# Kernel tuning notes

Measured on AMD Instinct MI355X. Metric: run time of the kernel, lower is better.

## Reference

```python
import jax, jax.numpy as jnp
import numpy as np

DIM = 1024
IMG_H, IMG_W = 512, 1408
CROP = 224
IMAGE_ORDER = (2, 0, 1, 5, 3, 4)
B, NC, NB = 2, 6, 32


def setup_inputs():
    key = jax.random.key(0)
    ks = jax.random.split(key, 12)
    camera_imgs = jax.random.normal(ks[0], (B, NC, 3, IMG_H, IMG_W), jnp.float32)
    u = jax.random.uniform(ks[1], (B, NB, 9), dtype=jnp.float32)
    centers = jnp.stack([u[..., 0] * 45.0 + 5.0,
                         (u[..., 1] - 0.5) * 40.0,
                         (u[..., 2] - 0.5) * 4.0], -1)
    pred_boxes = jnp.concatenate([centers, u[..., 3:] * 2.0], -1)  # [B,NB,9]
    K = np.array([[500., 0., IMG_W / 2.], [0., 500., IMG_H / 2.], [0., 0., 1.]])
    R_l2c = np.array([[0., -1., 0.], [0., 0., -1.], [1., 0., 0.]])  # lidar->camera axes
    mats = np.zeros((NC, 4, 4), np.float32)
    for c in range(NC):
        yaw = 2.0 * np.pi * c / NC
        Rz = np.array([[np.cos(yaw), -np.sin(yaw), 0.], [np.sin(yaw), np.cos(yaw), 0.], [0., 0., 1.]])
        mats[c, :3, :3] = K @ R_l2c @ Rz.T
        mats[c, 3, 3] = 1.0
    lidar2image = jnp.broadcast_to(jnp.asarray(mats), (B, NC, 4, 4))
    eye4 = jnp.eye(4, dtype=jnp.float32)
    img_aug_matrix = jnp.broadcast_to(eye4, (B, NC, 4, 4))
    lidar_aug_matrix = jnp.broadcast_to(eye4, (B, 4, 4))
    momentum = jnp.float32(0.5)
    box_default_dim = jax.random.normal(ks[2], (1, DIM), jnp.float32)
    theta_w = jnp.zeros((4, 9), jnp.float32)  # zero-init as in torch code
    theta_b = jnp.array([1., 0., 0., 1.], jnp.float32)

    def cw(k, shape):
        fan = shape[1] * shape[2] * shape[3]
        return jax.random.normal(k, shape, jnp.float32) * (2.0 / fan) ** 0.5
    conv1 = cw(ks[3], (64, 3, 7, 7))
    conv2 = cw(ks[4], (256, 64, 3, 3))
    conv3 = cw(ks[5], (DIM, 256, 3, 3))
    pos_embed = jax.random.normal(ks[6], (50, DIM), jnp.float32) * 0.02
    s = DIM ** -0.5
    wq = jax.random.normal(ks[7], (DIM, DIM), jnp.float32) * s
    wk = jax.random.normal(ks[8], (DIM, DIM), jnp.float32) * s
    wv = jax.random.normal(ks[9], (DIM, DIM), jnp.float32) * s
    wo = jax.random.normal(ks[10], (DIM, DIM), jnp.float32) * s
    return dict(camera_imgs=camera_imgs, pred_boxes=pred_boxes,
                img_aug_matrix=img_aug_matrix, lidar_aug_matrix=lidar_aug_matrix,
                lidar2image=lidar2image, momentum=momentum,
                box_default_dim=box_default_dim, theta_w=theta_w, theta_b=theta_b,
                conv1=conv1, conv2=conv2, conv3=conv3, pos_embed=pos_embed,
                wq=wq, wk=wk, wv=wv, wo=wo)


def _project(pred_boxes, lidar_aug_matrix, lidar2image, img_aug_matrix):
    # returns vu [B,NC,NB,2] = (row, col) pixel coords, on_img [B,NC,NB]
    def per_b(boxes, la, l2i, aug):
        c = boxes[:, :3] - la[:3, 3]                       # [NB,3]
        c = jnp.linalg.inv(la[:3, :3]) @ c.T               # [3,NB]
        c = l2i[:, :3, :3] @ c + l2i[:, :3, 3:4]           # [NC,3,NB]
        z = jnp.clip(c[:, 2], 1e-5, 1e5)
        xy = c[:, :2] / z[:, None]
        c = jnp.concatenate([xy, z[:, None]], 1)
        c = aug[:, :3, :3] @ c + aug[:, :3, 3:4]
        uv = c[:, :2].transpose(0, 2, 1)                   # [NC,NB,2] (col,row)
        vu = uv[..., ::-1]                                 # (row,col)
        on = (vu[..., 0] < IMG_H) & (vu[..., 0] >= 0) & (vu[..., 1] < IMG_W) & (vu[..., 1] >= 0)
        return vu, on
    return jax.vmap(per_b)(pred_boxes, lidar_aug_matrix, lidar2image, img_aug_matrix)


def _base_grid(h, w):
    # torch affine_grid align_corners=False pixel-center coords
    xs = (2.0 * jnp.arange(w) + 1.0) / w - 1.0
    ys = (2.0 * jnp.arange(h) + 1.0) / h - 1.0
    gx, gy = jnp.meshgrid(xs, ys)  # [h,w]
    return jnp.stack([gx, gy, jnp.ones_like(gx)], -1)  # [h,w,3]


def _grid_sample(img, grid):
    # img [C,H,W]; grid [...,2] xy in [-1,1]; bilinear, zeros padding, align_corners=False
    C, H, W = img.shape
    ix = ((grid[..., 0] + 1.0) * W - 1.0) / 2.0
    iy = ((grid[..., 1] + 1.0) * H - 1.0) / 2.0
    x0 = jnp.floor(ix); y0 = jnp.floor(iy)
    x1 = x0 + 1.0; y1 = y0 + 1.0
    wx = ix - x0; wy = iy - y0

    def gather(xx, yy):
        xi = jnp.clip(xx, 0, W - 1).astype(jnp.int32)
        yi = jnp.clip(yy, 0, H - 1).astype(jnp.int32)
        valid = (xx >= 0) & (xx <= W - 1) & (yy >= 0) & (yy <= H - 1)
        return img[:, yi, xi] * valid.astype(img.dtype)  # [C, ...]
    v00 = gather(x0, y0); v01 = gather(x1, y0)
    v10 = gather(x0, y1); v11 = gather(x1, y1)
    return (v00 * (1 - wx) * (1 - wy) + v01 * wx * (1 - wy)
            + v10 * (1 - wx) * wy + v11 * wx * wy)  # [C, ...]


def _clip_head(x, conv1, conv2, conv3, pos_embed, wq, wk, wv, wo):
    dn = ('NCHW', 'OIHW', 'NCHW')
    h = jax.nn.relu(jax.lax.conv_general_dilated(x, conv1, (4, 4), 'SAME', dimension_numbers=dn))
    h = jax.nn.relu(jax.lax.conv_general_dilated(h, conv2, (4, 4), 'SAME', dimension_numbers=dn))
    h = jax.nn.relu(jax.lax.conv_general_dilated(h, conv3, (2, 2), 'SAME', dimension_numbers=dn))  # [M,D,7,7]
    tok = h.reshape(h.shape[0], DIM, 49).transpose(0, 2, 1)              # [M,49,D]
    tok = jnp.concatenate([tok.mean(1, keepdims=True), tok], 1) + pos_embed  # [M,50,D]
    q = tok[:, :1] @ wq
    k = tok @ wk
    v = tok @ wv
    attn = jax.nn.softmax((q @ k.transpose(0, 2, 1)) * (DIM ** -0.5), -1)
    return ((attn @ v) @ wo)[:, 0]  # [M,D]


def reference(camera_imgs, pred_boxes, img_aug_matrix, lidar_aug_matrix, lidar2image,
              momentum, box_default_dim, theta_w, theta_b,
              conv1, conv2, conv3, pos_embed, wq, wk, wv, wo):
    N = B * NB
    vu, on_img = _project(pred_boxes, lidar_aug_matrix, lidar2image, img_aug_matrix)  # [B,NC,NB,2],[B,NC,NB]
    boxes_flat = pred_boxes.reshape(N, 9)
    rot = jnp.tanh(boxes_flat @ theta_w.T + theta_b).reshape(N, 2, 2)   # theta_rot MLP
    ty = vu[..., 0] / IMG_H * 2.0 - 1.0                                 # [B,NC,NB]
    tx = vu[..., 1] / IMG_W * 2.0 - 1.0
    pos = jnp.stack([tx, ty], -1).transpose(0, 2, 1, 3).reshape(N, NC, 2)
    theta = jnp.concatenate([jnp.broadcast_to(rot[:, None], (N, NC, 2, 2)),
                             pos[..., None]], -1)                        # [N,NC,2,3]
    base = _base_grid(CROP, CROP)                                        # [224,224,3]
    grids = jnp.einsum('hwk,ncjk->nchwj', base, theta)                   # [N,NC,224,224,2]
    grids = grids.reshape(B, NB, NC, CROP, CROP, 2)
    crops = []
    for b in range(B):
        for c in range(NC):
            smp = _grid_sample(camera_imgs[b, c], grids[b, :, c])        # [3,NB,224,224]
            crops.append(smp.transpose(1, 0, 2, 3))
    crops = jnp.stack(crops).reshape(B, NC, NB, 3, CROP, CROP)
    crops = crops.transpose(0, 2, 1, 3, 4, 5).reshape(N * NC, 3, CROP, CROP)
    emb = _clip_head(crops, conv1, conv2, conv3, pos_embed, wq, wk, wv, wo).reshape(N, NC, DIM)
    valid = on_img.transpose(0, 2, 1).reshape(N, NC)
    e = jnp.broadcast_to(box_default_dim, (N, DIM))
    for c in IMAGE_ORDER:  # sequential EMA over cameras, skipping off-image ones
        m = valid[:, c:c + 1]
        e = jnp.where(m, momentum * e + (1.0 - momentum) * emb[:, c], e)
    return e  # [N, DIM]
```

## Files before the change

kernel.cpp:

```cpp
#include <hip/hip_runtime.h>
#include <hip/hip_bf16.h>

#define DIMN 1024
#define IMG_H 512
#define IMG_W 1408
#define CROPN 224
#define NCAM 6
#define NBOXB 32
#define NBOX 64
#define NIMG 384

typedef __hip_bfloat16 bf16;
typedef unsigned short u16;
typedef float f32x4 __attribute__((ext_vector_type(4)));
typedef short bf16x8 __attribute__((ext_vector_type(8)));
typedef u16 u16x4 __attribute__((ext_vector_type(4)));
typedef u16 u16x8 __attribute__((ext_vector_type(8)));

__device__ __forceinline__ float b2f(bf16 x) { return __bfloat162float(x); }
__device__ __forceinline__ u16 f2us(float x) {
  bf16 h = __float2bfloat16(x);
  return *(u16*)&h;
}
__device__ __forceinline__ bf16x8 as_b(u16x8 x) {
  union { u16x8 u; bf16x8 b; } c; c.u = x; return c.b;
}

__global__ void k_w1r(const float* __restrict__ in, u16* __restrict__ out) {
  int idx = blockIdx.x * 256 + threadIdx.x;
  if (idx >= 64 * 224) return;
  int oc = idx / 224, t = idx % 224;
  int r = t >> 5, u = t & 31, kw = u >> 2, ch = u & 3;
  u16 v = (kw < 7 && ch < 3) ? f2us(in[((oc * 3 + ch) * 7 + r) * 7 + kw]) : (u16)0;
  out[(((oc >> 4) * 28 + (t >> 3)) * 16 + (oc & 15)) * 8 + (t & 7)] = v;
}
__global__ void k_w2r(const float* __restrict__ in, u16* __restrict__ out) {
  int idx = blockIdx.x * 256 + threadIdx.x;
  if (idx >= 256 * 576) return;
  int oc = idx / 576, t = idx % 576;
  int rk = t >> 6, ic = t & 63, r = rk / 3, kw = rk % 3;
  u16 v = f2us(in[((oc * 64 + ic) * 3 + r) * 3 + kw]);
  out[(((oc >> 4) * 72 + (t >> 3)) * 16 + (oc & 15)) * 8 + (t & 7)] = v;
}
__global__ void k_w3r(const float* __restrict__ in, u16* __restrict__ out) {
  int idx = blockIdx.x * 256 + threadIdx.x;
  if (idx >= 1024 * 2304) return;
  int oc = idx / 2304, t = idx % 2304;
  int rk = t >> 8, ic = t & 255, r = rk / 3, kw = rk % 3;
  u16 v = f2us(in[((oc * 256 + ic) * 3 + r) * 3 + kw]);
  int ocb = oc >> 4, mm = oc & 15, kb = t >> 3, kj = t & 7;
  out[(((size_t)ocb * 288 + kb) * 16 + mm) * 8 + kj] = v;
}
__global__ void k_transpose_t(const float* __restrict__ w, float* __restrict__ wt) {
  __shared__ float tile[32][33];
  int x = blockIdx.x * 32 + threadIdx.x;
  for (int j = threadIdx.y; j < 32; j += 8)
    tile[j][threadIdx.x] = w[(size_t)(blockIdx.y * 32 + j) * 1024 + x];
  __syncthreads();
  int x2 = blockIdx.y * 32 + threadIdx.x;
  for (int j = threadIdx.y; j < 32; j += 8)
    wt[(size_t)(blockIdx.x * 32 + j) * 1024 + x2] = tile[threadIdx.x][j];
}

__global__ void k_proj(const float* __restrict__ boxes, const float* __restrict__ la_m,
                       const float* __restrict__ l2i, const float* __restrict__ aug,
                       const float* __restrict__ tw, const float* __restrict__ tb,
                       float* __restrict__ theta_out, int* __restrict__ valid_out) {
  int t = threadIdx.x;
  if (t >= NIMG) return;
  int n = t / NCAM, cam = t % NCAM;
  int b = n / NBOXB, nb = n % NBOXB;

  float la[4][4];
  for (int r = 0; r < 4; r++)
    for (int c = 0; c < 4; c++) la[r][c] = la_m[b * 16 + r * 4 + c];
  float a00=la[0][0],a01=la[0][1],a02=la[0][2];
  float a10=la[1][0],a11=la[1][1],a12=la[1][2];
  float a20=la[2][0],a21=la[2][1],a22=la[2][2];
  float c00 =  a11*a22 - a12*a21;
  float c01 = -(a10*a22 - a12*a20);
  float c02 =  a10*a21 - a11*a20;
  float det = a00*c00 + a01*c01 + a02*c02;
  float id = 1.0f / det;
  float inv[3][3];
  inv[0][0] = c00*id;                 inv[0][1] = -(a01*a22-a02*a21)*id;  inv[0][2] =  (a01*a12-a02*a11)*id;
  inv[1][0] = c01*id;                 inv[1][1] =  (a00*a22-a02*a20)*id;  inv[1][2] = -(a00*a12-a02*a10)*id;
  inv[2][0] = c02*id;                 inv[2][1] = -(a00*a21-a01*a20)*id;  inv[2][2] =  (a00*a11-a01*a10)*id;

  float bx[9];
  for (int i = 0; i < 9; i++) bx[i] = boxes[(b * NBOXB + nb) * 9 + i];
  float c0[3] = { bx[0]-la[0][3], bx[1]-la[1][3], bx[2]-la[2][3] };
  float c1[3];
  for (int r = 0; r < 3; r++) c1[r] = inv[r][0]*c0[0] + inv[r][1]*c0[1] + inv[r][2]*c0[2];

  const float* M = l2i + (size_t)(b * NCAM + cam) * 16;
  float p[3];
  for (int r = 0; r < 3; r++)
    p[r] = M[r*4+0]*c1[0] + M[r*4+1]*c1[1] + M[r*4+2]*c1[2] + M[r*4+3];
  float z = fminf(fmaxf(p[2], 1e-5f), 100000.0f);
  float x = p[0] / z, y = p[1] / z;
  const float* A = aug + (size_t)(b * NCAM + cam) * 16;
  float u = A[0]*x + A[1]*y + A[2]*z + A[3];
  float v = A[4]*x + A[5]*y + A[6]*z + A[7];

  int on = (v < (float)IMG_H) && (v >= 0.0f) && (u < (float)IMG_W) && (u >= 0.0f);
  float ty = v / (float)IMG_H * 2.0f - 1.0f;
  float tx = u / (float)IMG_W * 2.0f - 1.0f;

  float s[4];
  for (int j = 0; j < 4; j++) {
    float acc = tb[j];
    for (int i = 0; i < 9; i++) acc += tw[j * 9 + i] * bx[i];
    s[j] = tanhf(acc);
  }
  float* o = theta_out + t * 6;
  o[0] = s[0]; o[1] = s[1]; o[2] = tx;
  o[3] = s[2]; o[4] = s[3]; o[5] = ty;
  valid_out[t] = on;
}

#define HALO_PX 1356
__global__ void k_zero_halo(u16x4* __restrict__ c) {
  int t = blockIdx.x * 256 + threadIdx.x;
  int i = t / HALO_PX;
  if (i >= NIMG) return;
  int r = t % HALO_PX;
  int ph, pw;
  if (r < 684) {
    int rr = r / 228;
    ph = (rr == 0) ? 0 : (rr == 1 ? 225 : 226);
    pw = r % 228;
  } else {
    int q = r - 684;
    ph = 1 + q / 3;
    int s = q % 3;
    pw = (s == 0) ? 0 : (s == 1 ? 225 : 226);
  }
  c[(size_t)i * 228 * 228 + ph * 228 + pw] = (u16x4){0, 0, 0, 0};
}

__global__ __launch_bounds__(256) void k_sample(const float* __restrict__ imgs,
                                                const float* __restrict__ theta,
                                                u16* __restrict__ crops) {
  int idx = blockIdx.x * 256 + threadIdx.x;
  int i = idx / (CROPN * CROPN);
  int rem = idx - i * (CROPN * CROPN);
  int yy = rem / CROPN, xx = rem % CROPN;
  const float* th = theta + i * 6;
  float gx = (2.0f * xx + 1.0f) / (float)CROPN - 1.0f;
  float gy = (2.0f * yy + 1.0f) / (float)CROPN - 1.0f;
  float grid_x = th[0]*gx + th[1]*gy + th[2];
  float grid_y = th[3]*gx + th[4]*gy + th[5];
  float ix = ((grid_x + 1.0f) * (float)IMG_W - 1.0f) * 0.5f;
  float iy = ((grid_y + 1.0f) * (float)IMG_H - 1.0f) * 0.5f;
  float x0 = floorf(ix), y0 = floorf(iy);
  float wx = ix - x0, wy = iy - y0;
  int cam = i % NCAM, b = i / (NBOXB * NCAM);
  const float* base = imgs + (size_t)(b * NCAM + cam) * 3 * IMG_H * IMG_W;

  float xf[2] = { x0, x0 + 1.0f };
  float yf[2] = { y0, y0 + 1.0f };
  float wxa[2] = { 1.0f - wx, wx };
  float wya[2] = { 1.0f - wy, wy };
  int   xi[2], yi[2], vx[2], vy[2];
  for (int j = 0; j < 2; j++) {
    vx[j] = (xf[j] >= 0.0f) && (xf[j] <= (float)(IMG_W - 1));
    vy[j] = (yf[j] >= 0.0f) && (yf[j] <= (float)(IMG_H - 1));
    xi[j] = (int)fminf(fmaxf(xf[j], 0.0f), (float)(IMG_W - 1));
    yi[j] = (int)fminf(fmaxf(yf[j], 0.0f), (float)(IMG_H - 1));
  }
  float res[3];
  #pragma unroll
  for (int ch = 0; ch < 3; ch++) {
    const float* cp = base + (size_t)ch * IMG_H * IMG_W;
    float r = 0.0f;
    #pragma unroll
    for (int jy = 0; jy < 2; jy++)
      #pragma unroll
      for (int jx = 0; jx < 2; jx++) {
        float val = (vx[jx] && vy[jy]) ? cp[yi[jy] * IMG_W + xi[jx]] : 0.0f;
        r += val * wxa[jx] * wya[jy];
      }
    res[ch] = r;
  }
  u16x4 st = { f2us(res[0]), f2us(res[1]), f2us(res[2]), 0 };
  *(u16x4*)(crops + ((size_t)i * 228 * 228 + (size_t)(yy + 1) * 228 + (xx + 1)) * 4) = st;
}


#define C1_GROUPS 34
__global__ __launch_bounds__(256) void k_conv1m(const u16* __restrict__ X,
                                                const u16* __restrict__ W,
                                                u16* __restrict__ out) {
  __shared__ u16x8 sX[C1_GROUPS * 64];
  int blk = blockIdx.x;
  int i = blk / 14, rg = blk % 14;
  int tid = threadIdx.x, wv = tid >> 6, lane = tid & 63;
  int m = lane & 15, quad = lane >> 4;

  const u16* src = X + ((size_t)i * 51984 + (size_t)(rg * 16) * 228) * 4;
  #pragma unroll
  for (int j = 0; j < 9; j++) {
    int g = wv + j * 4;
    if (g < C1_GROUPS) {
      int c = g * 64 + lane;
      int cc = c < 2166 ? c : 2165;
      __builtin_amdgcn_global_load_lds(
          (const __attribute__((address_space(1))) void*)(src + (size_t)cc * 8),
          (__attribute__((address_space(3))) void*)(sX + g * 64),
          16, 0, 0);
    }
  }
  __syncthreads();

  int col[4];
  #pragma unroll
  for (int nt = 0; nt < 4; nt++) col[nt] = nt * 16 + m;
  f32x4 acc[4][4];
  #pragma unroll
  for (int t = 0; t < 4; t++)
    #pragma unroll
    for (int nt = 0; nt < 4; nt++) acc[t][nt] = (f32x4){0.f, 0.f, 0.f, 0.f};

  #pragma unroll
  for (int r = 0; r < 7; r++) {
    bf16x8 a[4];
    #pragma unroll
    for (int t = 0; t < 4; t++)
      a[t] = as_b(*(const u16x8*)(W + (size_t)(((t * 28 + r * 4 + quad) * 16 + m) * 8)));
    int lrow = wv * 4 + r;
    #pragma unroll
    for (int nt = 0; nt < 4; nt++) {
      int cl = col[nt] < 56 ? col[nt] : 55;
      bf16x8 bfr = as_b(sX[lrow * 114 + cl * 2 + quad]);
      #pragma unroll
      for (int t = 0; t < 4; t++)
        acc[t][nt] = __builtin_amdgcn_mfma_f32_16x16x32_bf16(a[t], bfr, acc[t][nt], 0, 0, 0);
    }
  }
  int oh = rg * 4 + wv;
  #pragma unroll
  for (int nt = 0; nt < 4; nt++) {
    if (col[nt] < 56) {
      int n = oh * 56 + col[nt];
      #pragma unroll
      for (int t = 0; t < 4; t++) {
        u16x4 st;
        #pragma unroll
        for (int r4 = 0; r4 < 4; r4++) st[r4] = f2us(fmaxf(acc[t][nt][r4], 0.f));
        *(u16x4*)(out + ((size_t)i * 3136 + n) * 64 + t * 16 + quad * 4) = st;
      }
    }
  }
}

__global__ __launch_bounds__(256, 3) void k_conv2m(const u16* __restrict__ X,
                                                   const u16* __restrict__ W,
                                                   u16* __restrict__ out) {
  __shared__ u16x8 s2[3136];
  int bid = blockIdx.x;
  int i = bid / 7, ohg = bid % 7;
  int tid = threadIdx.x, wv = tid >> 6, lane = tid & 63;
  int m = lane & 15, quad = lane >> 4;

  const u16* src = X + ((size_t)i * 3136 + 8 * ohg * 56) * 64;
  u16x8 tmp[13];
  #pragma unroll
  for (int j = 0; j < 13; j++) {
    int c = tid + j * 256;
    int cc = c < 3136 ? c : 3135;
    tmp[j] = *(const u16x8*)(src + (size_t)cc * 8);
  }
  #pragma unroll
  for (int j = 0; j < 13; j++) {
    int c = tid + j * 256;
    int cc = c < 3136 ? c : 3135;
    int pixel = cc >> 3;
    int li = pixel / 56, iw = pixel - li * 56;
    int g = (14 * (li >> 2) + (iw >> 2)) & 15;
    s2[(cc & ~15) | ((cc ^ g) & 15)] = tmp[j];
  }
  __syncthreads();

  int nl[2], pk2[9][2];
  #pragma unroll
  for (int nt = 0; nt < 2; nt++) {
    int n = nt * 16 + m;
    nl[nt] = n;
    int nc = n < 28 ? n : 27;
    int ohl = nc / 14, ow = nc - ohl * 14;
    int g = nc & 15;
    #pragma unroll
    for (int rk = 0; rk < 9; rk++) {
      int r = rk / 3, kw = rk % 3;
      int pixel = (ohl * 4 + r) * 56 + (ow * 4 + kw);
      int cb = pixel * 8;
      int base2 = (cb & ~15) | ((cb & 8) ^ (g & 8));
      pk2[rk][nt] = base2 | (g & 7);
    }
  }
  f32x4 acc[4][2];
  #pragma unroll
  for (int t = 0; t < 4; t++)
    #pragma unroll
    for (int nt = 0; nt < 2; nt++) acc[t][nt] = (f32x4){0.f, 0.f, 0.f, 0.f};

  const u16* wbase = W + (size_t)(wv * 4) * (72 * 128) + m * 8;
  auto loadA = [&](int t, int s) {
    return as_b(*(const u16x8*)(wbase + (size_t)(t * 72 + s * 4 + quad) * 128));
  };
  auto loadB = [&](int nt, int s) {
    int pkv = pk2[s >> 1][nt];
    int sub = (s & 1) * 4 + quad;
    return as_b(s2[(pkv & ~7) | (sub ^ (pkv & 7))]);
  };

  bf16x8 A_[3][4], B_[3][2];
  #pragma unroll
  for (int t = 0; t < 4; t++) { A_[0][t] = loadA(t, 0); A_[1][t] = loadA(t, 1); }
  #pragma unroll
  for (int nt = 0; nt < 2; nt++) { B_[0][nt] = loadB(nt, 0); B_[1][nt] = loadB(nt, 1); }

  #pragma unroll
  for (int s = 0; s < 18; s++) {
    if (s + 2 < 18) {
      #pragma unroll
      for (int t = 0; t < 4; t++) A_[(s + 2) % 3][t] = loadA(t, s + 2);
      #pragma unroll
      for (int nt = 0; nt < 2; nt++) B_[(s + 2) % 3][nt] = loadB(nt, s + 2);
    }
    #pragma unroll
    for (int nt = 0; nt < 2; nt++)
      #pragma unroll
      for (int t = 0; t < 4; t++)
        acc[t][nt] = __builtin_amdgcn_mfma_f32_16x16x32_bf16(A_[s % 3][t], B_[s % 3][nt], acc[t][nt], 0, 0, 0);
  }

  #pragma unroll
  for (int nt = 0; nt < 2; nt++) {
    if (nl[nt] < 28) {
      int n = ohg * 28 + nl[nt];
      #pragma unroll
      for (int t = 0; t < 4; t++) {
        u16x4 st;
        #pragma unroll
        for (int r4 = 0; r4 < 4; r4++) st[r4] = f2us(fmaxf(acc[t][nt][r4], 0.f));
        *(u16x4*)(out + ((size_t)i * 196 + n) * 256 + wv * 64 + t * 16 + quad * 4) = st;
      }
    }
  }
}

__global__ __launch_bounds__(512, 2) void k_conv3m(const u16* __restrict__ X,
                                                   const u16* __restrict__ W,
                                                   float* __restrict__ out3) {
  __shared__ u16x8 sX8[6688];
  int bid = blockIdx.x;
  int og = (bid >> 2) & 1;
  int i  = (bid >> 3) * 4 + (bid & 3);
  int tid = threadIdx.x;
  int wv = tid >> 6, lane = tid & 63;

  const u16* src = X + (size_t)i * (196 * 256);
  #pragma unroll
  for (int j = 0; j < 13; j++) {
    int gi = (j < 12) ? (wv + j * 8) : (96 + wv);
    if (j < 12 || wv < 2) {
      int slot = gi * 64 + lane;
      int p = slot >> 5;
      int ih = p / 14, iw = p - ih * 14;
      int g = (7 * (ih >> 1) + (iw >> 1)) & 15;
      int c = (slot & ~15) | ((slot ^ g) & 15);
      __builtin_amdgcn_global_load_lds(
          (const __attribute__((address_space(1))) void*)(src + (size_t)c * 8),
          (__attribute__((address_space(3))) void*)(sX8 + gi * 64),
          16, 0, 0);
    }
  }
  if (tid < 32) sX8[6656 + tid] = (u16x8){0,0,0,0,0,0,0,0};
  __syncthreads();

  int m = lane & 15, quad = lane >> 4;
  int ocw = og * 512 + wv * 64;
  int narr[4], oh2[4], ow2[4];
  #pragma unroll
  for (int nt = 0; nt < 4; nt++) {
    int n = nt * 16 + m;
    narr[nt] = n;
    int nc = n < 49 ? n : 48;
    int oh = nc / 7, ow = nc - oh * 7;
    oh2[nt] = oh * 2; ow2[nt] = ow * 2;
  }
  f32x4 acc[4][4];
  #pragma unroll
  for (int t = 0; t < 4; t++)
    #pragma unroll
    for (int nt = 0; nt < 4; nt++) acc[t][nt] = (f32x4){0.f, 0.f, 0.f, 0.f};

  const u16* wbase = W + (size_t)(ocw >> 4) * (288 * 128) + m * 8;

  int bc[4], bk[4];
  auto set_bparams = [&](int rk) {
    const int r = rk / 3, kw = rk % 3;
    #pragma unroll
    for (int nt = 0; nt < 4; nt++) {
      int ih = oh2[nt] + r, iw = ow2[nt] + kw;
      bool valid = (narr[nt] < 49) && (ih < 14) && (iw < 14);
      int p = ih * 14 + iw;
      bc[nt] = valid ? p * 32 : 6656;
      bk[nt] = valid ? ((7 * (ih >> 1) + (iw >> 1)) & 15) : 0;
    }
  };
  auto loadA = [&](int t, int s) {
    return as_b(*(const u16x8*)(wbase + (size_t)(t * 288 + 4 * s + quad) * 128));
  };
  auto loadB = [&](int nt, int q4) {
    return as_b(sX8[bc[nt] + ((q4 + quad) ^ bk[nt])]);
  };

  bf16x8 A_[3][4], B_[2][4];
  set_bparams(0);
  #pragma unroll
  for (int t = 0; t < 4; t++) {
    A_[0][t] = loadA(t, 0);
    A_[1][t] = loadA(t, 1);
  }
  #pragma unroll
  for (int nt = 0; nt < 4; nt++) B_[0][nt] = loadB(nt, 0);

  #pragma unroll
  for (int s = 0; s < 72; s++) {
    if (s + 2 < 72) {
      #pragma unroll
      for (int t = 0; t < 4; t++) A_[(s + 2) % 3][t] = loadA(t, s + 2);
    }
    if (s + 1 < 72) {
      if (((s + 1) & 7) == 0) set_bparams((s + 1) >> 3);
      #pragma unroll
      for (int nt = 0; nt < 4; nt++) B_[(s + 1) & 1][nt] = loadB(nt, ((s + 1) & 7) * 4);
    }
    #pragma unroll
    for (int nt = 0; nt < 4; nt++)
      #pragma unroll
      for (int t = 0; t < 4; t++)
        acc[t][nt] = __builtin_amdgcn_mfma_f32_16x16x32_bf16(A_[s % 3][t], B_[s & 1][nt], acc[t][nt], 0, 0, 0);
  }

  #pragma unroll
  for (int nt = 0; nt < 4; nt++) {
    int n = narr[nt];
    if (n < 49) {
      #pragma unroll
      for (int t = 0; t < 4; t++) {
        f32x4 o;
        #pragma unroll
        for (int r4 = 0; r4 < 4; r4++) o[r4] = fmaxf(acc[t][nt][r4], 0.f);
        *(f32x4*)(out3 + ((size_t)i * 49 + n) * DIMN + ocw + t * 16 + quad * 4) = o;
      }
    }
  }
}

__global__ __launch_bounds__(256) void k_tok(const float* __restrict__ h,
                                             const float* __restrict__ pos,
                                             float* __restrict__ tok) {
  int blk = blockIdx.x;
  int i = blk / 50, t = blk % 50;
  int d = threadIdx.x * 4;
  float4 val;
  if (t == 0) {
    float sx = 0, sy = 0, sz = 0, sw = 0;
    for (int p = 0; p < 49; p++) {
      float4 v = *(const float4*)(h + ((size_t)i * 49 + p) * DIMN + d);
      sx += v.x; sy += v.y; sz += v.z; sw += v.w;
    }
    const float inv49 = 1.0f / 49.0f;
    val.x = sx * inv49; val.y = sy * inv49; val.z = sz * inv49; val.w = sw * inv49;
  } else {
    val = *(const float4*)(h + ((size_t)i * 49 + (t - 1)) * DIMN + d);
  }
  float4 pe = *(const float4*)(pos + (size_t)t * DIMN + d);
  float4 o; o.x = val.x + pe.x; o.y = val.y + pe.y; o.z = val.z + pe.z; o.w = val.w + pe.w;
  *(float4*)(tok + ((size_t)i * 50 + t) * DIMN + d) = o;
}

__global__ __launch_bounds__(256) void k_matvec2(const float* __restrict__ vecs, int vstride,
                                                 const float* __restrict__ M,
                                                 float* __restrict__ out) {
  __shared__ float s_v[4][DIMN];
  int i0 = blockIdx.x * 4;
  int h = blockIdx.y;
  for (int e = threadIdx.x; e < 4 * DIMN; e += 256)
    s_v[e >> 10][e & 1023] = vecs[(size_t)(i0 + (e >> 10)) * vstride + (e & 1023)];
  __syncthreads();
  int d0 = h * 512 + threadIdx.x * 2;
  float2 acc[4] = {{0,0},{0,0},{0,0},{0,0}};
  for (int e = 0; e < DIMN; e++) {
    float2 w = *(const float2*)(M + (size_t)e * DIMN + d0);
    #pragma unroll
    for (int im = 0; im < 4; im++) {
      float x = s_v[im][e];
      acc[im].x += x * w.x; acc[im].y += x * w.y;
    }
  }
  #pragma unroll
  for (int im = 0; im < 4; im++)
    *(float2*)(out + (size_t)(i0 + im) * DIMN + d0) = acc[im];
}

__global__ __launch_bounds__(256) void k_attn(const float* __restrict__ tok,
                                              const float* __restrict__ a1,
                                              float* __restrict__ tvec) {
  __shared__ float s_a[DIMN];
  __shared__ float s_sc[50];
  __shared__ float s_at[50];
  int i = blockIdx.x;
  for (int e = threadIdx.x; e < DIMN; e += 256) s_a[e] = a1[(size_t)i * DIMN + e];
  __syncthreads();
  int wave = threadIdx.x >> 6, lane = threadIdx.x & 63;
  for (int t = wave; t < 50; t += 4) {
    const float* tr = tok + ((size_t)i * 50 + t) * DIMN;
    float p = 0.0f;
    for (int mm = 0; mm < 16; mm++) {
      int e = lane + mm * 64;
      p += tr[e] * s_a[e];
    }
    for (int off = 32; off > 0; off >>= 1) p += __shfl_down(p, off, 64);
    if (lane == 0) s_sc[t] = p * 0.03125f;
  }
  __syncthreads();
  if (threadIdx.x == 0) {
    float mx = s_sc[0];
    for (int t = 1; t < 50; t++) mx = fmaxf(mx, s_sc[t]);
    float sum = 0.0f;
    for (int t = 0; t < 50; t++) { float ex = expf(s_sc[t] - mx); s_at[t] = ex; sum += ex; }
    float inv = 1.0f / sum;
    for (int t = 0; t < 50; t++) s_at[t] *= inv;
  }
  __syncthreads();
  int d0 = threadIdx.x * 4;
  float ax = 0, ay = 0, az = 0, aw = 0;
  for (int t = 0; t < 50; t++) {
    float at = s_at[t];
    float4 tv = *(const float4*)(tok + ((size_t)i * 50 + t) * DIMN + d0);
    ax += at * tv.x; ay += at * tv.y; az += at * tv.z; aw += at * tv.w;
  }
  float4 o; o.x = ax; o.y = ay; o.z = az; o.w = aw;
  *(float4*)(tvec + (size_t)i * DIMN + d0) = o;
}

__global__ void k_final(const float* __restrict__ emb,
                        const int* __restrict__ valid,
                        const float* __restrict__ bdd,
                        const float* __restrict__ momp,
                        float* __restrict__ out) {
  int n = blockIdx.x;
  int d0 = threadIdx.x * 4;
  float mom = momp[0];
  float e[4];
  #pragma unroll
  for (int j = 0; j < 4; j++) e[j] = bdd[d0 + j];
  const int order[6] = {2, 0, 1, 5, 3, 4};
  #pragma unroll
  for (int s = 0; s < 6; s++) {
    int c = order[s];
    int i = n * NCAM + c;
    if (valid[i]) {
      const float* er = emb + (size_t)i * DIMN + d0;
      #pragma unroll
      for (int j = 0; j < 4; j++) e[j] = mom * e[j] + (1.0f - mom) * er[j];
    }
  }
  #pragma unroll
  for (int j = 0; j < 4; j++) out[(size_t)n * DIMN + d0 + j] = e[j];
}

extern "C" void kernel_launch(void* const* d_in, const int* in_sizes, int n_in,
                              void* d_out, int out_size, void* d_ws, size_t ws_size,
                              hipStream_t stream) {
  const float* in_cam = (const float*)d_in[0];
  const float* in_box = (const float*)d_in[1];
  const float* in_aug = (const float*)d_in[2];
  const float* in_la  = (const float*)d_in[3];
  const float* in_l2i = (const float*)d_in[4];
  const float* in_mom = (const float*)d_in[5];
  const float* in_bdd = (const float*)d_in[6];
  const float* in_tw  = (const float*)d_in[7];
  const float* in_tb  = (const float*)d_in[8];
  const float* in_c1  = (const float*)d_in[9];
  const float* in_c2  = (const float*)d_in[10];
  const float* in_c3  = (const float*)d_in[11];
  const float* in_pe  = (const float*)d_in[12];
  const float* in_wq  = (const float*)d_in[13];
  const float* in_wk  = (const float*)d_in[14];
  const float* in_wv  = (const float*)d_in[15];
  const float* in_wo  = (const float*)d_in[16];

  char* base = (char*)d_ws;
  size_t off = 0;
  auto carve = [&](size_t bytes) -> char* {
    char* p = base + off;
    off += (bytes + 255) & ~(size_t)255;
    return p;
  };
  float* theta   = (float*)carve((size_t)NIMG * 6 * 4);
  int*   valid   = (int*)carve((size_t)NIMG * 4);
  float* qbuf    = (float*)carve((size_t)NIMG * DIMN * 4);
  float* a1buf   = (float*)carve((size_t)NIMG * DIMN * 4);
  float* tvbuf   = (float*)carve((size_t)NIMG * DIMN * 4);
  float* ctxbuf  = (float*)carve((size_t)NIMG * DIMN * 4);
  float* embbuf  = (float*)carve((size_t)NIMG * DIMN * 4);
  float* wkT_f   = (float*)carve((size_t)DIMN * DIMN * 4);
  u16*   W1r     = (u16*)carve((size_t)64 * 224 * 2);
  u16*   W2r     = (u16*)carve((size_t)256 * 576 * 2);
  u16*   W3r     = (u16*)carve((size_t)1024 * 2304 * 2);
  u16*   c2o     = (u16*)carve((size_t)NIMG * 196 * 256 * 2);
  char*  R1      = carve((size_t)NIMG * 228 * 228 * 4 * 2);
  u16*   c1o     = (u16*)carve((size_t)NIMG * 3136 * 64 * 2);
  u16*   crops   = (u16*)R1;
  float* conv3o  = (float*)R1;
  float* tok     = (float*)(R1 + (size_t)NIMG * 49 * DIMN * 4);

  k_w1r<<<56, 256, 0, stream>>>(in_c1, W1r);
  k_w2r<<<576, 256, 0, stream>>>(in_c2, W2r);
  k_w3r<<<9216, 256, 0, stream>>>(in_c3, W3r);
  k_transpose_t<<<dim3(32, 32), dim3(32, 8), 0, stream>>>(in_wk, wkT_f);

  k_proj<<<1, 384, 0, stream>>>(in_box, in_la, in_l2i, in_aug, in_tw, in_tb, theta, valid);
  k_zero_halo<<<(NIMG * HALO_PX + 255) / 256, 256, 0, stream>>>((u16x4*)crops);
  k_sample<<<(NIMG * CROPN * CROPN) / 256, 256, 0, stream>>>(in_cam, theta, crops);
  k_conv1m<<<NIMG * 14, 256, 0, stream>>>(crops, W1r, c1o);
  k_conv2m<<<NIMG * 7, 256, 0, stream>>>(c1o, W2r, c2o);
  k_conv3m<<<768, 512, 0, stream>>>(c2o, W3r, conv3o);
  k_tok<<<NIMG * 50, 256, 0, stream>>>(conv3o, in_pe, tok);
  k_matvec2<<<dim3(96, 2), 256, 0, stream>>>(tok, 50 * DIMN, in_wq, qbuf);
  k_matvec2<<<dim3(96, 2), 256, 0, stream>>>(qbuf, DIMN, wkT_f, a1buf);
  k_attn<<<NIMG, 256, 0, stream>>>(tok, a1buf, tvbuf);
  k_matvec2<<<dim3(96, 2), 256, 0, stream>>>(tvbuf, DIMN, in_wv, ctxbuf);
  k_matvec2<<<dim3(96, 2), 256, 0, stream>>>(ctxbuf, DIMN, in_wo, embbuf);
  k_final<<<NBOX, 256, 0, stream>>>(embbuf, valid, in_bdd, in_mom, (float*)d_out);
}
```

Measured before the change: 937.4 us.

## Restructure conv3 blocks to process two images per block with split-K LDS staging

Each conv3 block now covers two images and a quarter of the output channels, where before it covered one image and half the channels. Four waves serve each image, and the input channels are staged into LDS in two halves, so the shared buffer holds both images at half depth. The aim is to reuse each weight fragment load across two images and halve weight traffic per output. In exchange there are extra barriers between the halves, and the staging of the second half is not overlapped with compute.

```diff
diff --git a/kernel.cpp b/kernel.cpp
--- a/kernel.cpp
+++ b/kernel.cpp
@@ -354,34 +354,43 @@
 __global__ __launch_bounds__(512, 2) void k_conv3m(const u16* __restrict__ X,
                                                    const u16* __restrict__ W,
                                                    float* __restrict__ out3) {
-  __shared__ u16x8 sX8[6688];
+  __shared__ u16x8 sX8[6288];
   int bid = blockIdx.x;
-  int og = (bid >> 2) & 1;
-  int i  = (bid >> 3) * 4 + (bid & 3);
+  int og = (bid >> 1) & 3;
+  int pair = (bid >> 3) * 2 + (bid & 1);
+  int i0 = pair * 2;
   int tid = threadIdx.x;
   int wv = tid >> 6, lane = tid & 63;
 
-  const u16* src = X + (size_t)i * (196 * 256);
-  #pragma unroll
-  for (int j = 0; j < 13; j++) {
-    int gi = (j < 12) ? (wv + j * 8) : (96 + wv);
-    if (j < 12 || wv < 2) {
-      int slot = gi * 64 + lane;
-      int p = slot >> 5;
-      int ih = p / 14, iw = p - ih * 14;
-      int g = (7 * (ih >> 1) + (iw >> 1)) & 15;
-      int c = (slot & ~15) | ((slot ^ g) & 15);
-      __builtin_amdgcn_global_load_lds(
-          (const __attribute__((address_space(1))) void*)(src + (size_t)c * 8),
-          (__attribute__((address_space(3))) void*)(sX8 + gi * 64),
-          16, 0, 0);
-    }
-  }
-  if (tid < 32) sX8[6656 + tid] = (u16x8){0,0,0,0,0,0,0,0};
-  __syncthreads();
+  const u16* srcb = X + (size_t)i0 * 50176;
+
+  auto stage = [&](int h) {
+    #pragma unroll
+    for (int j = 0; j < 13; j++) {
+      int gi = (j < 12) ? (wv + j * 8) : (96 + wv);
+      if (j < 12 || wv < 2) {
+        int slot = gi * 64 + lane;
+        int simg = slot >= 3136 ? 1 : 0;
+        int local = slot - simg * 3136;
+        int p = local >> 4, cq = local & 15;
+        int ih = p / 14, iw = p - ih * 14;
+        int g = (7 * (ih >> 1) + (iw >> 1)) & 15;
+        size_t gc = (size_t)simg * 6272 + (size_t)p * 32 + h * 16 + (cq ^ g);
+        __builtin_amdgcn_global_load_lds(
+            (const __attribute__((address_space(1))) void*)(srcb + gc * 8),
+            (__attribute__((address_space(3))) void*)(sX8 + gi * 64),
+            16, 0, 0);
+      }
+    }
+  };
+
+  stage(0);
+  if (tid < 16) sX8[6272 + tid] = (u16x8){0,0,0,0,0,0,0,0};
 
   int m = lane & 15, quad = lane >> 4;
-  int ocw = og * 512 + wv * 64;
+  int ocw = og * 256 + (wv & 3) * 64;
+  int imgb = (wv >> 2) * 3136;
+  int iimg = i0 + (wv >> 2);
   int narr[4], oh2[4], ow2[4];
   #pragma unroll
   for (int nt = 0; nt < 4; nt++) {
@@ -407,43 +416,51 @@
       int ih = oh2[nt] + r, iw = ow2[nt] + kw;
       bool valid = (narr[nt] < 49) && (ih < 14) && (iw < 14);
       int p = ih * 14 + iw;
-      bc[nt] = valid ? p * 32 : 6656;
+      bc[nt] = valid ? (imgb + p * 16) : 6272;
       bk[nt] = valid ? ((7 * (ih >> 1) + (iw >> 1)) & 15) : 0;
     }
   };
-  auto loadA = [&](int t, int s) {
-    return as_b(*(const u16x8*)(wbase + (size_t)(t * 288 + 4 * s + quad) * 128));
+  auto loadA = [&](int t, int s, int h) {
+    int kblk = (s >> 2) * 32 + h * 16 + (s & 3) * 4 + quad;
+    return as_b(*(const u16x8*)(wbase + (size_t)(t * 288 + kblk) * 128));
   };
-  auto loadB = [&](int nt, int q4) {
-    return as_b(sX8[bc[nt] + ((q4 + quad) ^ bk[nt])]);
+  auto loadB = [&](int nt, int s) {
+    int q = (s & 3) * 4 + quad;
+    return as_b(sX8[bc[nt] + (q ^ bk[nt])]);
   };
 
   bf16x8 A_[3][4], B_[2][4];
-  set_bparams(0);
-  #pragma unroll
-  for (int t = 0; t < 4; t++) {
-    A_[0][t] = loadA(t, 0);
-    A_[1][t] = loadA(t, 1);
-  }
-  #pragma unroll
-  for (int nt = 0; nt < 4; nt++) B_[0][nt] = loadB(nt, 0);
-
-  #pragma unroll
-  for (int s = 0; s < 72; s++) {
-    if (s + 2 < 72) {
-      #pragma unroll
-      for (int t = 0; t < 4; t++) A_[(s + 2) % 3][t] = loadA(t, s + 2);
-    }
-    if (s + 1 < 72) {
-      if (((s + 1) & 7) == 0) set_bparams((s + 1) >> 3);
-      #pragma unroll
-      for (int nt = 0; nt < 4; nt++) B_[(s + 1) & 1][nt] = loadB(nt, ((s + 1) & 7) * 4);
-    }
-    #pragma unroll
-    for (int nt = 0; nt < 4; nt++)
-      #pragma unroll
-      for (int t = 0; t < 4; t++)
-        acc[t][nt] = __builtin_amdgcn_mfma_f32_16x16x32_bf16(A_[s % 3][t], B_[s & 1][nt], acc[t][nt], 0, 0, 0);
+
+  #pragma unroll
+  for (int h = 0; h < 2; h++) {
+    __syncthreads();
+    set_bparams(0);
+    #pragma unroll
+    for (int t = 0; t < 4; t++) { A_[0][t] = loadA(t, 0, h); A_[1][t] = loadA(t, 1, h); }
+    #pragma unroll
+    for (int nt = 0; nt < 4; nt++) B_[0][nt] = loadB(nt, 0);
+
+    #pragma unroll
+    for (int s = 0; s < 36; s++) {
+      if (s + 2 < 36) {
+        #pragma unroll
+        for (int t = 0; t < 4; t++) A_[(s + 2) % 3][t] = loadA(t, s + 2, h);
+      }
+      if (s + 1 < 36) {
+        if (((s + 1) & 3) == 0) set_bparams((s + 1) >> 2);
+        #pragma unroll
+        for (int nt = 0; nt < 4; nt++) B_[(s + 1) & 1][nt] = loadB(nt, s + 1);
+      }
+      #pragma unroll
+      for (int nt = 0; nt < 4; nt++)
+        #pragma unroll
+        for (int t = 0; t < 4; t++)
+          acc[t][nt] = __builtin_amdgcn_mfma_f32_16x16x32_bf16(A_[s % 3][t], B_[s & 1][nt], acc[t][nt], 0, 0, 0);
+    }
+    if (h == 0) {
+      __syncthreads();
+      stage(1);
+    }
   }
 
   #pragma unroll
@@ -455,7 +472,7 @@
         f32x4 o;
         #pragma unroll
         for (int r4 = 0; r4 < 4; r4++) o[r4] = fmaxf(acc[t][nt][r4], 0.f);
-        *(f32x4*)(out3 + ((size_t)i * 49 + n) * DIMN + ocw + t * 16 + quad * 4) = o;
+        *(f32x4*)(out3 + ((size_t)iimg * 49 + n) * DIMN + ocw + t * 16 + quad * 4) = o;
       }
     }
   }
```

Result: no change. 939.1 us (+0.2%).
